# Kernel optimization log

Measured on AMD Instinct MI355X. Metric: run time of the kernel, lower is better.

Reference implementation:

```python
import jax, jax.numpy as jnp
import numpy as np

N, T, D_ENC, D_DEC, U = 32, 2048, 1024, 1024, 1024


def setup_inputs() -> dict:
    key = jax.random.key(0)
    k1, k2, k3, k4, k5, k6 = jax.random.split(key, 6)
    queries = jax.random.normal(k1, (N, 1, D_DEC), dtype=jnp.float32)
    encoder_output = jax.random.normal(k2, (N, T, D_ENC), dtype=jnp.float32)
    # lengths in [1, T] so every row has at least one valid position
    lengths = jax.random.randint(k3, (N,), 1, T + 1, dtype=jnp.int32)
    v = jax.random.normal(k4, (U,), dtype=jnp.float32)
    # torch Linear weights are [out, in]; y = x @ W.T
    Wq = jax.random.normal(k5, (U, D_DEC), dtype=jnp.float32) * (1.0 / np.sqrt(D_DEC))
    Wk = jax.random.normal(k6, (U, D_ENC), dtype=jnp.float32) * (1.0 / np.sqrt(D_ENC))
    return {"queries": queries, "encoder_output": encoder_output,
            "lengths": lengths, "v": v, "Wq": Wq, "Wk": Wk}


def reference(queries, encoder_output, lengths, v, Wq, Wk):
    # set_memory: project keys, build padding mask
    proj_key = jnp.einsum('nte,ue->ntu', encoder_output, Wk)      # [N,T,U]
    mask = jnp.arange(T)[None, :] >= lengths[:, None]             # [N,T] True = masked

    # forward (normalize=False path)
    proj_query = jnp.einsum('nqd,ud->nqu', queries, Wq)           # [N,1,U]
    weights = jnp.tanh(proj_query + proj_key) @ v                 # [N,T]
    weights = jnp.where(mask, -jnp.inf, weights)
    alignments = jax.nn.softmax(weights, axis=-1)                 # [N,T]
    contexts = jnp.einsum('nt,nte->ne', alignments, encoder_output)  # [N,D_enc]
    return contexts, alignments
```

## Files before the change

### kernel.cpp

```cpp
#include <hip/hip_runtime.h>
#include <hip/hip_bf16.h>

#define NB 32
#define TD 2048
#define DIM 1024

typedef _Float16 v8h __attribute__((ext_vector_type(8)));
typedef _Float16 v4h __attribute__((ext_vector_type(4)));
typedef float    v4f __attribute__((ext_vector_type(4)));

__device__ __forceinline__ float ftanh(float x) {
    x = fminf(15.f, fmaxf(-15.f, x));
    float e = __expf(2.f * x);
    return (e - 1.f) / (e + 1.f);
}

__device__ __forceinline__ void gld_lds16(const void* g, void* l) {
    __builtin_amdgcn_global_load_lds(
        (const __attribute__((address_space(1))) unsigned int*)g,
        (__attribute__((address_space(3))) unsigned int*)l, 16, 0, 0);
}

__global__ __launch_bounds__(256) void pq_kernel(const float* __restrict__ q,
                                                 const float* __restrict__ Wq,
                                                 float* __restrict__ pq) {
    int wid  = blockIdx.x * 4 + (threadIdx.x >> 6);
    int lane = threadIdx.x & 63;
    int n = wid >> 10;
    int u = wid & 1023;
    const float4* qr = (const float4*)(q  + (size_t)n * DIM);
    const float4* wr = (const float4*)(Wq + (size_t)u * DIM);
    float s = 0.f;
#pragma unroll
    for (int j = 0; j < 4; ++j) {
        int i = lane + 64 * j;
        float4 a = qr[i], b = wr[i];
        s += a.x * b.x + a.y * b.y + a.z * b.z + a.w * b.w;
    }
#pragma unroll
    for (int off = 32; off >= 1; off >>= 1) s += __shfl_xor(s, off);
    if (lane == 0) pq[(size_t)n * DIM + u] = s;
}

__global__ __launch_bounds__(256) void cvt_kernel(const float* __restrict__ enc,
                                                  const float* __restrict__ Wk,
                                                  const int* __restrict__ lengths,
                                                  _Float16* __restrict__ ench,
                                                  _Float16* __restrict__ wkh) {
    int local = threadIdx.x * 8;
    int rsub  = local >> 10;
    int col   = local & 1023;
    const float* src;
    _Float16* dst;
    size_t row;
    if (blockIdx.x < 32768) {
        row = (size_t)blockIdx.x * 2 + rsub;
        int n = (int)(row >> 11), t = (int)(row & 2047);
        if (t >= lengths[n]) return;
        src = enc; dst = ench;
    } else {
        row = (size_t)(blockIdx.x - 32768) * 2 + rsub;
        src = Wk; dst = wkh;
    }
    const float4* s = (const float4*)(src + row * DIM + col);
    float4 a = s[0], b = s[1];
    v8h h;
    h[0] = (_Float16)a.x; h[1] = (_Float16)a.y; h[2] = (_Float16)a.z; h[3] = (_Float16)a.w;
    h[4] = (_Float16)b.x; h[5] = (_Float16)b.y; h[6] = (_Float16)b.z; h[7] = (_Float16)b.w;
    *(v8h*)(dst + row * DIM + col) = h;
}

__global__ __launch_bounds__(256) void gemm_tanh_h3(
        const _Float16* __restrict__ ench, const _Float16* __restrict__ wkh,
        const float* __restrict__ pq, const float* __restrict__ v,
        const int* __restrict__ lengths, float* __restrict__ weights) {
    const int bid = blockIdx.x;
    const int xcd = bid & 7;
    const int idx = bid >> 3;
    const int bm  = ((idx >> 3) << 3) | xcd;
    const int bn  = idx & 7;
    const int rowBase = bm * 128;
    const int n = rowBase >> 11;
    const int tstart = rowBase & 2047;
    if (lengths[n] <= tstart) return;

    __shared__ _Float16 As[128 * 64];
    __shared__ _Float16 Bs[128 * 64];

    const int tid  = threadIdx.x;
    const int lane = tid & 63;
    const int wv   = tid >> 6;
    const int wm   = wv >> 1, wn = wv & 1;
    const int q4   = lane >> 4;
    const int l16  = lane & 15;

    const int sr  = lane >> 3;
    const int scs = (lane & 7) ^ sr;

    const _Float16* Ag = ench + (size_t)(rowBase + wv * 32 + sr) * DIM + scs * 8;
    const _Float16* Bg = wkh + (size_t)(bn * 128 + wv * 32 + sr) * DIM + scs * 8;
    _Float16* Al = &As[(wv * 32) * 64];
    _Float16* Bl = &Bs[(wv * 32) * 64];

    v4f acc[4][4];
    const v4f vz = {0.f, 0.f, 0.f, 0.f};
#pragma unroll
    for (int i = 0; i < 4; ++i)
#pragma unroll
        for (int j = 0; j < 4; ++j) acc[i][j] = vz;

    for (int k0 = 0; k0 < DIM; k0 += 64) {
        __syncthreads();
#pragma unroll
        for (int j = 0; j < 4; ++j) {
            gld_lds16(Ag + k0 + j * 8 * DIM, Al + j * 8 * 64);
            gld_lds16(Bg + k0 + j * 8 * DIM, Bl + j * 8 * 64);
        }
        __syncthreads();

#pragma unroll
        for (int kk = 0; kk < 2; ++kk) {
            v8h a[4], b[4];
#pragma unroll
            for (int mt = 0; mt < 4; ++mt) {
                int r = wm * 64 + mt * 16 + l16;
                a[mt] = *(const v8h*)(&As[r * 64 + (((kk * 4 + q4) ^ (r & 7)) * 8)]);
            }
#pragma unroll
            for (int nt = 0; nt < 4; ++nt) {
                int r = wn * 64 + nt * 16 + l16;
                b[nt] = *(const v8h*)(&Bs[r * 64 + (((kk * 4 + q4) ^ (r & 7)) * 8)]);
            }
#pragma unroll
            for (int mt = 0; mt < 4; ++mt)
#pragma unroll
                for (int nt = 0; nt < 4; ++nt)
                    acc[mt][nt] = __builtin_amdgcn_mfma_f32_16x16x32_f16(
                        a[mt], b[nt], acc[mt][nt], 0, 0, 0);
        }
    }

    float pqv[4], vv[4];
#pragma unroll
    for (int nt = 0; nt < 4; ++nt) {
        int ug = bn * 128 + wn * 64 + nt * 16 + l16;
        pqv[nt] = pq[(size_t)n * DIM + ug];
        vv[nt]  = v[ug];
    }
#pragma unroll
    for (int mt = 0; mt < 4; ++mt) {
#pragma unroll
        for (int r = 0; r < 4; ++r) {
            float s = 0.f;
#pragma unroll
            for (int nt = 0; nt < 4; ++nt)
                s += ftanh(acc[mt][nt][r] + pqv[nt]) * vv[nt];
            s += __shfl_xor(s, 1);
            s += __shfl_xor(s, 2);
            s += __shfl_xor(s, 4);
            s += __shfl_xor(s, 8);
            if (l16 == 0) {
                int R = rowBase + wm * 64 + mt * 16 + q4 * 4 + r;
                atomicAdd(&weights[R], s);
            }
        }
    }
}

__global__ __launch_bounds__(256) void gemm_tanh_kernel(
        const float* __restrict__ enc, const float* __restrict__ Wk,
        const float* __restrict__ pq,  const float* __restrict__ v,
        const int* __restrict__ lengths, float* __restrict__ weights) {
    const int bm = blockIdx.x;
    const int bn = blockIdx.y;
    const int rowBase = bm * 128;
    const int n = rowBase >> 11;
    const int tstart = rowBase & 2047;
    if (lengths[n] <= tstart) return;

    __shared__ _Float16 As[128 * 40];
    __shared__ _Float16 Bs[128 * 40];

    const int tid  = threadIdx.x;
    const int lane = tid & 63;
    const int wv   = tid >> 6;
    const int wm   = wv >> 1, wn = wv & 1;
    const int q4   = lane >> 4;
    const int l16  = lane & 15;

    v4f acc[4][4];
    const v4f vz = {0.f, 0.f, 0.f, 0.f};
#pragma unroll
    for (int i = 0; i < 4; ++i)
#pragma unroll
        for (int j = 0; j < 4; ++j) acc[i][j] = vz;

    const int srow = tid >> 3;
    const int skc  = (tid & 7) * 4;

    for (int k0 = 0; k0 < DIM; k0 += 32) {
        __syncthreads();
#pragma unroll
        for (int j = 0; j < 4; ++j) {
            int row = j * 32 + srow;
            float4 av = *(const float4*)(enc + (size_t)(rowBase + row) * DIM + k0 + skc);
            v4h ah;
            ah.x = (_Float16)av.x; ah.y = (_Float16)av.y;
            ah.z = (_Float16)av.z; ah.w = (_Float16)av.w;
            *(v4h*)(&As[row * 40 + skc]) = ah;
            float4 bv = *(const float4*)(Wk + (size_t)(bn * 128 + row) * DIM + k0 + skc);
            v4h bh;
            bh.x = (_Float16)bv.x; bh.y = (_Float16)bv.y;
            bh.z = (_Float16)bv.z; bh.w = (_Float16)bv.w;
            *(v4h*)(&Bs[row * 40 + skc]) = bh;
        }
        __syncthreads();

        v8h afr[4], bfr[4];
#pragma unroll
        for (int mt = 0; mt < 4; ++mt)
            afr[mt] = *(const v8h*)(&As[(wm * 64 + mt * 16 + l16) * 40 + q4 * 8]);
#pragma unroll
        for (int nt = 0; nt < 4; ++nt)
            bfr[nt] = *(const v8h*)(&Bs[(wn * 64 + nt * 16 + l16) * 40 + q4 * 8]);
#pragma unroll
        for (int mt = 0; mt < 4; ++mt)
#pragma unroll
            for (int nt = 0; nt < 4; ++nt)
                acc[mt][nt] = __builtin_amdgcn_mfma_f32_16x16x32_f16(
                    afr[mt], bfr[nt], acc[mt][nt], 0, 0, 0);
    }

    float pqv[4], vv[4];
#pragma unroll
    for (int nt = 0; nt < 4; ++nt) {
        int ug = bn * 128 + wn * 64 + nt * 16 + l16;
        pqv[nt] = pq[(size_t)n * DIM + ug];
        vv[nt]  = v[ug];
    }
#pragma unroll
    for (int mt = 0; mt < 4; ++mt) {
#pragma unroll
        for (int r = 0; r < 4; ++r) {
            float s = 0.f;
#pragma unroll
            for (int nt = 0; nt < 4; ++nt)
                s += ftanh(acc[mt][nt][r] + pqv[nt]) * vv[nt];
            s += __shfl_xor(s, 1);
            s += __shfl_xor(s, 2);
            s += __shfl_xor(s, 4);
            s += __shfl_xor(s, 8);
            if (l16 == 0) {
                int R = rowBase + wm * 64 + mt * 16 + q4 * 4 + r;
                atomicAdd(&weights[R], s);
            }
        }
    }
}

__global__ __launch_bounds__(256) void softmax_kernel(float* __restrict__ w,
                                                      const int* __restrict__ lengths) {
    int n = blockIdx.x;
    int len = lengths[n];
    float* row = w + (size_t)n * TD;
    int tid = threadIdx.x;
    float wv[8], ev[8];
    float mx = -INFINITY;
#pragma unroll
    for (int i = 0; i < 8; ++i) {
        int t = tid + i * 256;
        float x = row[t];
        x = (t < len) ? x : -INFINITY;
        wv[i] = x;
        mx = fmaxf(mx, x);
    }
#pragma unroll
    for (int off = 32; off >= 1; off >>= 1) mx = fmaxf(mx, __shfl_xor(mx, off));
    __shared__ float redm[4], reds[4];
    int lane = tid & 63, wvid = tid >> 6;
    if (lane == 0) redm[wvid] = mx;
    __syncthreads();
    mx = fmaxf(fmaxf(redm[0], redm[1]), fmaxf(redm[2], redm[3]));
    float sm = 0.f;
#pragma unroll
    for (int i = 0; i < 8; ++i) { ev[i] = __expf(wv[i] - mx); sm += ev[i]; }
#pragma unroll
    for (int off = 32; off >= 1; off >>= 1) sm += __shfl_xor(sm, off);
    if (lane == 0) reds[wvid] = sm;
    __syncthreads();
    sm = reds[0] + reds[1] + reds[2] + reds[3];
    float inv = 1.f / sm;
#pragma unroll
    for (int i = 0; i < 8; ++i) row[tid + i * 256] = ev[i] * inv;
}

__global__ __launch_bounds__(256) void ctx_kernel_h3(const float* __restrict__ align,
                                                     const _Float16* __restrict__ ench,
                                                     const int* __restrict__ lengths,
                                                     float* __restrict__ ctx) {
    int n  = blockIdx.y;
    int t0 = blockIdx.x * 128;
    int len = lengths[n];
    if (len <= t0) return;
    int half = threadIdx.x >> 7;
    int col  = (threadIdx.x & 127) * 8;
    float acc[8];
#pragma unroll
    for (int i = 0; i < 8; ++i) acc[i] = 0.f;
    int tend = min(t0 + 128, len);
    const float* arow = align + (size_t)n * TD;
    const _Float16* ebase = ench + (size_t)n * TD * DIM + col;
    for (int t = t0 + half; t < tend; t += 2) {
        float a = arow[t];
        v8h e = *(const v8h*)(ebase + (size_t)t * DIM);
#pragma unroll
        for (int i = 0; i < 8; ++i) acc[i] += a * (float)e[i];
    }
    __shared__ float cred[DIM];
    if (half == 1) {
#pragma unroll
        for (int i = 0; i < 8; ++i) cred[col + i] = acc[i];
    }
    __syncthreads();
    if (half == 0) {
        float* c = ctx + (size_t)n * DIM + col;
#pragma unroll
        for (int i = 0; i < 8; ++i) atomicAdd(c + i, acc[i] + cred[col + i]);
    }
}

__global__ __launch_bounds__(256) void ctx_kernel(const float* __restrict__ align,
                                                  const float* __restrict__ enc,
                                                  const int* __restrict__ lengths,
                                                  float* __restrict__ ctx) {
    int n  = blockIdx.y;
    int t0 = blockIdx.x * 128;
    if (lengths[n] <= t0) return;
    int e = threadIdx.x * 4;
    float4 acc = make_float4(0.f, 0.f, 0.f, 0.f);
    const float* arow = align + (size_t)n * TD;
    const float* erow = enc + (size_t)n * TD * DIM;
    for (int tt = 0; tt < 128; ++tt) {
        int t = t0 + tt;
        float a = arow[t];
        if (a != 0.f) {
            float4 evv = *(const float4*)(erow + (size_t)t * DIM + e);
            acc.x += a * evv.x; acc.y += a * evv.y;
            acc.z += a * evv.z; acc.w += a * evv.w;
        }
    }
    float* c = ctx + (size_t)n * DIM + e;
    atomicAdd(c + 0, acc.x);
    atomicAdd(c + 1, acc.y);
    atomicAdd(c + 2, acc.z);
    atomicAdd(c + 3, acc.w);
}

extern "C" void kernel_launch(void* const* d_in, const int* in_sizes, int n_in,
                              void* d_out, int out_size, void* d_ws, size_t ws_size,
                              hipStream_t stream) {
    const float* queries = (const float*)d_in[0];
    const float* enc     = (const float*)d_in[1];
    const int*   lengths = (const int*)d_in[2];
    const float* v       = (const float*)d_in[3];
    const float* Wq      = (const float*)d_in[4];
    const float* Wk      = (const float*)d_in[5];

    float* out = (float*)d_out;
    float* ctx = out;
    float* alg = out + NB * DIM;
    float* pq  = ctx;
    (void)in_sizes; (void)n_in; (void)out_size;

    const size_t ench_elems = (size_t)NB * TD * DIM;
    const size_t need = (ench_elems + (size_t)DIM * DIM) * sizeof(_Float16);

    hipMemsetAsync(alg, 0, (size_t)NB * TD * sizeof(float), stream);
    pq_kernel<<<NB * DIM / 4, 256, 0, stream>>>(queries, Wq, pq);

    if (ws_size >= need) {
        _Float16* ench = (_Float16*)d_ws;
        _Float16* wkh  = ench + ench_elems;
        cvt_kernel<<<32768 + 512, 256, 0, stream>>>(enc, Wk, lengths, ench, wkh);
        gemm_tanh_h3<<<4096, 256, 0, stream>>>(ench, wkh, pq, v, lengths, alg);
        softmax_kernel<<<NB, 256, 0, stream>>>(alg, lengths);
        hipMemsetAsync(ctx, 0, (size_t)NB * DIM * sizeof(float), stream);
        ctx_kernel_h3<<<dim3(16, NB), 256, 0, stream>>>(alg, ench, lengths, ctx);
    } else {
        dim3 g2(512, 8);
        gemm_tanh_kernel<<<g2, 256, 0, stream>>>(enc, Wk, pq, v, lengths, alg);
        softmax_kernel<<<NB, 256, 0, stream>>>(alg, lengths);
        hipMemsetAsync(ctx, 0, (size_t)NB * DIM * sizeof(float), stream);
        ctx_kernel<<<dim3(16, NB), 256, 0, stream>>>(alg, enc, lengths, ctx);
    }
}
```

Baseline: 517.7 us.

## Fuse query projection into conversion kernel and split context reduction finer

Folds the query projection into the fp16 conversion launch as 128 extra blocks, each reusing two Wq rows across all 32 batches, which removes one kernel launch and redundant Wq reads. The pq and v loads in the GEMM are moved ahead of the K loop to hide their latency. The context kernel now uses 64-timestep chunks with twice as many blocks and an unrolled loop, giving more parallelism at the cost of more atomic adds.

Result: no change. 522.0 us (+0.8%).

```diff
diff --git a/kernel.cpp b/kernel.cpp
--- a/kernel.cpp
+++ b/kernel.cpp
@@ -19,6 +19,70 @@
     __builtin_amdgcn_global_load_lds(
         (const __attribute__((address_space(1))) unsigned int*)g,
         (__attribute__((address_space(3))) unsigned int*)l, 16, 0, 0);
+}
+
+__global__ __launch_bounds__(256) void prep_kernel(
+        const float* __restrict__ enc, const float* __restrict__ Wk,
+        const float* __restrict__ queries, const float* __restrict__ Wq,
+        const int* __restrict__ lengths,
+        _Float16* __restrict__ ench, _Float16* __restrict__ wkh,
+        float* __restrict__ pq) {
+    int bid = blockIdx.x;
+    if (bid < 128) {
+        int lane = threadIdx.x & 63;
+        int wv   = threadIdx.x >> 6;
+        int u    = bid * 8 + wv * 2;
+        const float* w0 = Wq + (size_t)u * DIM;
+        const float* w1 = w0 + DIM;
+        float4 wq0[4], wq1[4];
+#pragma unroll
+        for (int j = 0; j < 4; ++j) {
+            wq0[j] = *(const float4*)(w0 + j * 256 + lane * 4);
+            wq1[j] = *(const float4*)(w1 + j * 256 + lane * 4);
+        }
+        for (int n = 0; n < NB; ++n) {
+            const float* qn = queries + (size_t)n * DIM;
+            float s0 = 0.f, s1 = 0.f;
+#pragma unroll
+            for (int j = 0; j < 4; ++j) {
+                float4 qv = *(const float4*)(qn + j * 256 + lane * 4);
+                s0 += qv.x * wq0[j].x + qv.y * wq0[j].y + qv.z * wq0[j].z + qv.w * wq0[j].w;
+                s1 += qv.x * wq1[j].x + qv.y * wq1[j].y + qv.z * wq1[j].z + qv.w * wq1[j].w;
+            }
+#pragma unroll
+            for (int off = 32; off >= 1; off >>= 1) {
+                s0 += __shfl_xor(s0, off);
+                s1 += __shfl_xor(s1, off);
+            }
+            if (lane == 0) {
+                pq[(size_t)n * DIM + u]     = s0;
+                pq[(size_t)n * DIM + u + 1] = s1;
+            }
+        }
+        return;
+    }
+    int cb = bid - 128;
+    int local = threadIdx.x * 8;
+    int rsub  = local >> 10;
+    int col   = local & 1023;
+    const float* src;
+    _Float16* dst;
+    size_t row;
+    if (cb < 32768) {
+        row = (size_t)cb * 2 + rsub;
+        int n = (int)(row >> 11), t = (int)(row & 2047);
+        if (t >= lengths[n]) return;
+        src = enc; dst = ench;
+    } else {
+        row = (size_t)(cb - 32768) * 2 + rsub;
+        src = Wk; dst = wkh;
+    }
+    const float4* s = (const float4*)(src + row * DIM + col);
+    float4 a = s[0], b = s[1];
+    v8h h;
+    h[0] = (_Float16)a.x; h[1] = (_Float16)a.y; h[2] = (_Float16)a.z; h[3] = (_Float16)a.w;
+    h[4] = (_Float16)b.x; h[5] = (_Float16)b.y; h[6] = (_Float16)b.z; h[7] = (_Float16)b.w;
+    *(v8h*)(dst + row * DIM + col) = h;
 }
 
 __global__ __launch_bounds__(256) void pq_kernel(const float* __restrict__ q,
@@ -40,34 +104,6 @@
 #pragma unroll
     for (int off = 32; off >= 1; off >>= 1) s += __shfl_xor(s, off);
     if (lane == 0) pq[(size_t)n * DIM + u] = s;
-}
-
-__global__ __launch_bounds__(256) void cvt_kernel(const float* __restrict__ enc,
-                                                  const float* __restrict__ Wk,
-                                                  const int* __restrict__ lengths,
-                                                  _Float16* __restrict__ ench,
-                                                  _Float16* __restrict__ wkh) {
-    int local = threadIdx.x * 8;
-    int rsub  = local >> 10;
-    int col   = local & 1023;
-    const float* src;
-    _Float16* dst;
-    size_t row;
-    if (blockIdx.x < 32768) {
-        row = (size_t)blockIdx.x * 2 + rsub;
-        int n = (int)(row >> 11), t = (int)(row & 2047);
-        if (t >= lengths[n]) return;
-        src = enc; dst = ench;
-    } else {
-        row = (size_t)(blockIdx.x - 32768) * 2 + rsub;
-        src = Wk; dst = wkh;
-    }
-    const float4* s = (const float4*)(src + row * DIM + col);
-    float4 a = s[0], b = s[1];
-    v8h h;
-    h[0] = (_Float16)a.x; h[1] = (_Float16)a.y; h[2] = (_Float16)a.z; h[3] = (_Float16)a.w;
-    h[4] = (_Float16)b.x; h[5] = (_Float16)b.y; h[6] = (_Float16)b.z; h[7] = (_Float16)b.w;
-    *(v8h*)(dst + row * DIM + col) = h;
 }
 
 __global__ __launch_bounds__(256) void gemm_tanh_h3(
@@ -94,6 +130,14 @@
     const int q4   = lane >> 4;
     const int l16  = lane & 15;
 
+    float pqv[4], vv[4];
+#pragma unroll
+    for (int nt = 0; nt < 4; ++nt) {
+        int ug = bn * 128 + wn * 64 + nt * 16 + l16;
+        pqv[nt] = pq[(size_t)n * DIM + ug];
+        vv[nt]  = v[ug];
+    }
+
     const int sr  = lane >> 3;
     const int scs = (lane & 7) ^ sr;
 
@@ -140,13 +184,6 @@
         }
     }
 
-    float pqv[4], vv[4];
-#pragma unroll
-    for (int nt = 0; nt < 4; ++nt) {
-        int ug = bn * 128 + wn * 64 + nt * 16 + l16;
-        pqv[nt] = pq[(size_t)n * DIM + ug];
-        vv[nt]  = v[ug];
-    }
 #pragma unroll
     for (int mt = 0; mt < 4; ++mt) {
 #pragma unroll
@@ -294,12 +331,12 @@
     for (int i = 0; i < 8; ++i) row[tid + i * 256] = ev[i] * inv;
 }
 
-__global__ __launch_bounds__(256) void ctx_kernel_h3(const float* __restrict__ align,
+__global__ __launch_bounds__(256) void ctx_kernel_h4(const float* __restrict__ align,
                                                      const _Float16* __restrict__ ench,
                                                      const int* __restrict__ lengths,
                                                      float* __restrict__ ctx) {
     int n  = blockIdx.y;
-    int t0 = blockIdx.x * 128;
+    int t0 = blockIdx.x * 64;
     int len = lengths[n];
     if (len <= t0) return;
     int half = threadIdx.x >> 7;
@@ -307,9 +344,10 @@
     float acc[8];
 #pragma unroll
     for (int i = 0; i < 8; ++i) acc[i] = 0.f;
-    int tend = min(t0 + 128, len);
+    int tend = min(t0 + 64, len);
     const float* arow = align + (size_t)n * TD;
     const _Float16* ebase = ench + (size_t)n * TD * DIM + col;
+#pragma unroll 2
     for (int t = t0 + half; t < tend; t += 2) {
         float a = arow[t];
         v8h e = *(const v8h*)(ebase + (size_t)t * DIM);
@@ -376,17 +414,18 @@
     const size_t need = (ench_elems + (size_t)DIM * DIM) * sizeof(_Float16);
 
     hipMemsetAsync(alg, 0, (size_t)NB * TD * sizeof(float), stream);
-    pq_kernel<<<NB * DIM / 4, 256, 0, stream>>>(queries, Wq, pq);
 
     if (ws_size >= need) {
         _Float16* ench = (_Float16*)d_ws;
         _Float16* wkh  = ench + ench_elems;
-        cvt_kernel<<<32768 + 512, 256, 0, stream>>>(enc, Wk, lengths, ench, wkh);
+        prep_kernel<<<128 + 32768 + 512, 256, 0, stream>>>(
+            enc, Wk, queries, Wq, lengths, ench, wkh, pq);
         gemm_tanh_h3<<<4096, 256, 0, stream>>>(ench, wkh, pq, v, lengths, alg);
         softmax_kernel<<<NB, 256, 0, stream>>>(alg, lengths);
         hipMemsetAsync(ctx, 0, (size_t)NB * DIM * sizeof(float), stream);
-        ctx_kernel_h3<<<dim3(16, NB), 256, 0, stream>>>(alg, ench, lengths, ctx);
+        ctx_kernel_h4<<<dim3(32, NB), 256, 0, stream>>>(alg, ench, lengths, ctx);
     } else {
+        pq_kernel<<<NB * DIM / 4, 256, 0, stream>>>(queries, Wq, pq);
         dim3 g2(512, 8);
         gemm_tanh_kernel<<<g2, 256, 0, stream>>>(enc, Wk, pq, v, lengths, alg);
         softmax_kernel<<<NB, 256, 0, stream>>>(alg, lengths);
```
